# Kernel optimization log

Measured on AMD Instinct MI355X. Metric: run time of the kernel, lower is better.

Reference implementation:

```python
import jax, jax.numpy as jnp
import numpy as np

E = 19   # electrodes
H = 32   # lstm hidden dim per direction


def setup_inputs() -> dict:
    key = jax.random.key(0)
    ks = jax.random.split(key, 8)
    B, T = 64, 2048
    s = 1.0 / np.sqrt(H)  # PyTorch LSTM/Linear init scale
    u = lambda k, shp: jax.random.uniform(k, shp, jnp.float32, -s, s)
    return {
        "x": jax.random.normal(ks[0], (B, T, E), jnp.float32),
        # per-electrode, per-direction LSTM params (input_dim=1 so w_ih is a vector per gate block)
        "w_ih": u(ks[1], (E, 2, 4 * H)),          # [E, dir, 4H]
        "w_hh": u(ks[2], (E, 2, 4 * H, H)),       # [E, dir, 4H, H]
        "b_ih": u(ks[3], (E, 2, 4 * H)),
        "b_hh": u(ks[4], (E, 2, 4 * H)),
        "ln_gamma": jnp.ones((E, 2 * H), jnp.float32),
        "ln_beta": jnp.zeros((E, 2 * H), jnp.float32),
        "fc_w": u(ks[5], (1, 2 * H)),
        "fc_b": u(ks[6], (1,)),
    }


def reference(x, w_ih, w_hh, b_ih, b_hh, ln_gamma, ln_beta, fc_w, fc_b):
    B, T, E_ = x.shape
    # dir 0 = forward time, dir 1 = reversed time (bidirectional)
    xs = jnp.stack([x, x[:, ::-1, :]], axis=-1)      # [B, T, E, 2]
    xs = jnp.moveaxis(xs, 1, 0)                      # [T, B, E, 2]
    b = b_ih + b_hh                                  # [E, 2, 4H]

    h0 = jnp.zeros((B, E_, 2, H), x.dtype)
    c0 = jnp.zeros_like(h0)

    def step(carry, xt):
        h, c = carry
        # xt: [B, E, 2] scalar input per electrode/direction (input_dim == 1)
        gates = xt[..., None] * w_ih + jnp.einsum('bedh,edgh->bedg', h, w_hh) + b
        i, f, g, o = jnp.split(gates, 4, axis=-1)    # PyTorch gate order i,f,g,o
        c = jax.nn.sigmoid(f) * c + jax.nn.sigmoid(i) * jnp.tanh(g)
        h = jax.nn.sigmoid(o) * jnp.tanh(c)
        return (h, c), None

    (hT, _), _ = jax.lax.scan(step, (h0, c0), xs)
    # final hidden: dir0 = fwd at t=T-1 (hn[-2]), dir1 = bwd at t=0 (hn[-1]); concat features
    out = hT.reshape(B, E_, 2 * H)                   # [B, E, 64]

    # per-electrode LayerNorm over the 64-dim feature
    mu = out.mean(-1, keepdims=True)
    var = out.var(-1, keepdims=True)
    out = (out - mu) / jnp.sqrt(var + 1e-5) * ln_gamma + ln_beta

    pooled = out.mean(axis=1)                        # mean over electrodes -> [B, 64]
    logits = pooled @ fc_w.T + fc_b                  # [B, 1]
    return logits[:, 0]
```

## Files before the change

kernel.cpp:

```cpp
#include <hip/hip_runtime.h>
#include <math.h>
#include <stdint.h>

#define E_N 19
#define H_N 32
#define T_N 2048
#define B_N 64
#define G_N 128
#define XCHUNK 32
#define LOG2E 1.4426950408889634f

typedef _Float16 half2_t __attribute__((ext_vector_type(2)));

__device__ __forceinline__ float sigm_rcp(float e) {
    return __builtin_amdgcn_rcpf(1.0f + e);
}

__global__ __launch_bounds__(64)
__attribute__((amdgpu_waves_per_eu(1, 1)))
void lstm_chain_kernel(
    const float* __restrict__ x,
    const float* __restrict__ w_ih,
    const float* __restrict__ w_hh,
    const float* __restrict__ b_ih,
    const float* __restrict__ b_hh,
    float* __restrict__ hT)
{
    const int lane = threadIdx.x;
    const int be   = blockIdx.x;
    const int b    = be / E_N;
    const int e    = be - b * E_N;
    const int j    = lane & 31;
    const int half = lane >> 5;
    const int ed   = e * 2 + half;

    const float* wbase = w_hh + (size_t)ed * G_N * H_N;
    uint32_t wp[4][16];
    #pragma unroll
    for (int r = 0; r < 4; ++r) {
        const float* wr = wbase + (size_t)(j + 32 * r) * H_N;
        #pragma unroll
        for (int m = 0; m < 16; ++m) {
            float2 v = ((const float2*)wr)[m];
            half2_t p = { (_Float16)v.x, (_Float16)v.y };
            wp[r][m] = __builtin_bit_cast(uint32_t, p);
        }
    }
    float wih[4], bias[4];
    #pragma unroll
    for (int r = 0; r < 4; ++r) {
        const int row = j + 32 * r;
        wih[r]  = w_ih[(size_t)ed * G_N + row];
        bias[r] = b_ih[(size_t)ed * G_N + row] + b_hh[(size_t)ed * G_N + row];
    }

    __shared__ __align__(16) uint16_t hbuf[64];
    __shared__ float xbuf[64];

    hbuf[lane] = 0;
    float c = 0.0f, h = 0.0f;

    const float* xbase = x + (size_t)b * T_N * E_N + e;

    float xreg;
    {
        const int tphys = half ? (T_N - 1 - j) : j;
        xreg = xbase[(size_t)tphys * E_N];
    }

    for (int t0 = 0; t0 < T_N; t0 += XCHUNK) {
        #pragma unroll
        for (int r = 0; r < 4; ++r)
            #pragma unroll
            for (int m = 0; m < 16; ++m)
                asm volatile("" : "+v"(wp[r][m]));

        xbuf[lane] = xreg;
        if (t0 + XCHUNK < T_N) {
            const int tn    = t0 + XCHUNK + j;
            const int tphys = half ? (T_N - 1 - tn) : tn;
            xreg = xbase[(size_t)tphys * E_N];
        }

        #pragma unroll 1
        for (int tl = 0; tl < XCHUNK; ++tl) {
            const uint4 q0 = ((const uint4*)hbuf)[half * 4 + 0];
            const uint4 q1 = ((const uint4*)hbuf)[half * 4 + 1];
            const uint4 q2 = ((const uint4*)hbuf)[half * 4 + 2];
            const uint4 q3 = ((const uint4*)hbuf)[half * 4 + 3];
            const float sx = xbuf[(half << 5) + tl];

            uint32_t hp[16];
            hp[0]=q0.x; hp[1]=q0.y; hp[2]=q0.z; hp[3]=q0.w;
            hp[4]=q1.x; hp[5]=q1.y; hp[6]=q1.z; hp[7]=q1.w;
            hp[8]=q2.x; hp[9]=q2.y; hp[10]=q2.z; hp[11]=q2.w;
            hp[12]=q3.x; hp[13]=q3.y; hp[14]=q3.z; hp[15]=q3.w;

            float acc[4], accb[4];
            #pragma unroll
            for (int r = 0; r < 4; ++r) {
                acc[r]  = fmaf(sx, wih[r], bias[r]);
                accb[r] = 0.0f;
            }
            #pragma unroll
            for (int m = 0; m < 8; ++m) {
                #pragma unroll
                for (int r = 0; r < 4; ++r) {
                    acc[r]  = __builtin_amdgcn_fdot2(
                        __builtin_bit_cast(half2_t, hp[m]),
                        __builtin_bit_cast(half2_t, wp[r][m]),   acc[r],  false);
                    accb[r] = __builtin_amdgcn_fdot2(
                        __builtin_bit_cast(half2_t, hp[m + 8]),
                        __builtin_bit_cast(half2_t, wp[r][m + 8]), accb[r], false);
                }
            }
            const float gi = acc[0] + accb[0];
            const float gf = acc[1] + accb[1];
            const float gg = acc[2] + accb[2];
            const float go = acc[3] + accb[3];

            const float si = sigm_rcp(__builtin_amdgcn_exp2f(gi * (-LOG2E)));
            const float sf = sigm_rcp(__builtin_amdgcn_exp2f(gf * (-LOG2E)));
            const float tg = fmaf(2.0f, sigm_rcp(
                __builtin_amdgcn_exp2f(gg * (-2.0f * LOG2E))), -1.0f);
            const float so = sigm_rcp(__builtin_amdgcn_exp2f(go * (-LOG2E)));

            c = fmaf(sf, c, si * tg);
            const float tc = fmaf(2.0f, sigm_rcp(
                __builtin_amdgcn_exp2f(c * (-2.0f * LOG2E))), -1.0f);
            h = so * tc;

            hbuf[lane] = __builtin_bit_cast(uint16_t, (_Float16)h);
        }
    }

    hT[((size_t)(b * E_N + e) * 2 + half) * H_N + j] = h;
}

__global__ __launch_bounds__(64) void head_kernel(
    const float* __restrict__ hT,
    const float* __restrict__ ln_gamma,
    const float* __restrict__ ln_beta,
    const float* __restrict__ fc_w,
    const float* __restrict__ fc_b,
    float* __restrict__ out)
{
    const int b = blockIdx.x;
    const int f = threadIdx.x;

    float acc = 0.0f;
    for (int e = 0; e < E_N; ++e) {
        const float v = hT[(size_t)(b * E_N + e) * 64 + f];
        float s = v, s2 = v * v;
        #pragma unroll
        for (int off = 32; off > 0; off >>= 1) {
            s  += __shfl_xor(s,  off);
            s2 += __shfl_xor(s2, off);
        }
        const float mean = s * (1.0f / 64.0f);
        const float var  = s2 * (1.0f / 64.0f) - mean * mean;
        const float inv  = rsqrtf(var + 1e-5f);
        acc += (v - mean) * inv * ln_gamma[e * 64 + f] + ln_beta[e * 64 + f];
    }
    float contrib = (acc * (1.0f / (float)E_N)) * fc_w[f];
    #pragma unroll
    for (int off = 32; off > 0; off >>= 1) contrib += __shfl_xor(contrib, off);
    if (f == 0) out[b] = contrib + fc_b[0];
}

extern "C" void kernel_launch(void* const* d_in, const int* in_sizes, int n_in,
                              void* d_out, int out_size, void* d_ws, size_t ws_size,
                              hipStream_t stream) {
    const float* x        = (const float*)d_in[0];
    const float* w_ih     = (const float*)d_in[1];
    const float* w_hh     = (const float*)d_in[2];
    const float* b_ih     = (const float*)d_in[3];
    const float* b_hh     = (const float*)d_in[4];
    const float* ln_gamma = (const float*)d_in[5];
    const float* ln_beta  = (const float*)d_in[6];
    const float* fc_w     = (const float*)d_in[7];
    const float* fc_b     = (const float*)d_in[8];
    float* out = (float*)d_out;
    float* hT  = (float*)d_ws;

    lstm_chain_kernel<<<B_N * E_N, 64, 0, stream>>>(x, w_ih, w_hh, b_ih, b_hh, hT);
    head_kernel<<<B_N, 64, 0, stream>>>(hT, ln_gamma, ln_beta, fc_w, fc_b, out);
}
```

Before: 1.093 ms.

## Batch 16 sequences per wave and compute LSTM recurrence with MFMA

Replaces the per-(batch, electrode) fdot2 recurrence with one wave per (electrode, direction, group of 16 batches). The hidden-state matvec becomes eight 16x16x32 f16 MFMAs per step. The accumulator layout is arranged so each lane's new h values land directly in the B-fragment, which removes the LDS round trip for h. The gate activation scales are folded into the weights and bias. The grid shrinks from 1216 to 152 waves, so throughput now depends on per-step MFMA and transcendental latency rather than on how many waves can run at once. Each lane also computes 32 sigmoids per step instead of 4.

```diff
diff --git a/kernel.cpp b/kernel.cpp
--- a/kernel.cpp
+++ b/kernel.cpp
@@ -7,10 +7,10 @@
 #define T_N 2048
 #define B_N 64
 #define G_N 128
-#define XCHUNK 32
 #define LOG2E 1.4426950408889634f
 
-typedef _Float16 half2_t __attribute__((ext_vector_type(2)));
+typedef _Float16 f16x8 __attribute__((ext_vector_type(8)));
+typedef float    f32x4 __attribute__((ext_vector_type(4)));
 
 __device__ __forceinline__ float sigm_rcp(float e) {
     return __builtin_amdgcn_rcpf(1.0f + e);
@@ -18,7 +18,7 @@
 
 __global__ __launch_bounds__(64)
 __attribute__((amdgpu_waves_per_eu(1, 1)))
-void lstm_chain_kernel(
+void lstm_mfma_kernel(
     const float* __restrict__ x,
     const float* __restrict__ w_ih,
     const float* __restrict__ w_hh,
@@ -27,114 +27,104 @@
     float* __restrict__ hT)
 {
     const int lane = threadIdx.x;
-    const int be   = blockIdx.x;
-    const int b    = be / E_N;
-    const int e    = be - b * E_N;
-    const int j    = lane & 31;
-    const int half = lane >> 5;
-    const int ed   = e * 2 + half;
+    const int blk  = blockIdx.x;
+    const int ed   = blk >> 2;
+    const int g    = blk & 3;
+    const int e    = ed >> 1;
+    const int d    = ed & 1;
+    const int q    = lane >> 4;
+    const int col  = lane & 15;
+    const int b    = g * 16 + col;
 
-    const float* wbase = w_hh + (size_t)ed * G_N * H_N;
-    uint32_t wp[4][16];
+    const float* whh = w_hh + (size_t)ed * G_N * H_N;
+    f16x8 av[8];
+    float biasv[32], wihv[32];
     #pragma unroll
-    for (int r = 0; r < 4; ++r) {
-        const float* wr = wbase + (size_t)(j + 32 * r) * H_N;
+    for (int m = 0; m < 8; ++m) {
+        const float sc = ((m >> 1) == 2) ? (-2.0f * LOG2E) : (-LOG2E);
+        {
+            const int t   = col;
+            const int row = 32 * (m >> 1) + 8 * (t >> 2) + (t & 3) + 4 * (m & 1);
+            const float* wr = whh + (size_t)row * H_N + q * 8;
+            #pragma unroll
+            for (int j = 0; j < 8; ++j) av[m][j] = (_Float16)(wr[j] * sc);
+        }
         #pragma unroll
-        for (int m = 0; m < 16; ++m) {
-            float2 v = ((const float2*)wr)[m];
-            half2_t p = { (_Float16)v.x, (_Float16)v.y };
-            wp[r][m] = __builtin_bit_cast(uint32_t, p);
+        for (int r = 0; r < 4; ++r) {
+            const int row = 32 * (m >> 1) + 8 * q + r + 4 * (m & 1);
+            biasv[m * 4 + r] = (b_ih[(size_t)ed * G_N + row] +
+                                b_hh[(size_t)ed * G_N + row]) * sc;
+            wihv[m * 4 + r]  = w_ih[(size_t)ed * G_N + row] * sc;
         }
     }
-    float wih[4], bias[4];
+
+    float cst[8], hout[8];
+    f16x8 bfrag;
     #pragma unroll
-    for (int r = 0; r < 4; ++r) {
-        const int row = j + 32 * r;
-        wih[r]  = w_ih[(size_t)ed * G_N + row];
-        bias[r] = b_ih[(size_t)ed * G_N + row] + b_hh[(size_t)ed * G_N + row];
+    for (int dd = 0; dd < 8; ++dd) {
+        cst[dd] = 0.0f; hout[dd] = 0.0f; bfrag[dd] = (_Float16)0.0f;
     }
 
-    __shared__ __align__(16) uint16_t hbuf[64];
-    __shared__ float xbuf[64];
-
-    hbuf[lane] = 0;
-    float c = 0.0f, h = 0.0f;
-
-    const float* xbase = x + (size_t)b * T_N * E_N + e;
-
-    float xreg;
-    {
-        const int tphys = half ? (T_N - 1 - j) : j;
-        xreg = xbase[(size_t)tphys * E_N];
+    const float* xb = x + (size_t)b * T_N * E_N + e;
+    float xc[4], xn[4];
+    #pragma unroll
+    for (int s = 0; s < 4; ++s) {
+        const int tp = d ? (T_N - 1 - s) : s;
+        xc[s] = xb[(size_t)tp * E_N];
     }
 
-    for (int t0 = 0; t0 < T_N; t0 += XCHUNK) {
+    #pragma unroll 1
+    for (int t0 = 0; t0 < T_N; t0 += 4) {
+        if (t0 + 4 < T_N) {
+            #pragma unroll
+            for (int s = 0; s < 4; ++s) {
+                const int tn = t0 + 4 + s;
+                const int tp = d ? (T_N - 1 - tn) : tn;
+                xn[s] = xb[(size_t)tp * E_N];
+            }
+        }
         #pragma unroll
-        for (int r = 0; r < 4; ++r)
+        for (int s = 0; s < 4; ++s) {
+            const float xv = xc[s];
+            f32x4 C[8];
             #pragma unroll
-            for (int m = 0; m < 16; ++m)
-                asm volatile("" : "+v"(wp[r][m]));
-
-        xbuf[lane] = xreg;
-        if (t0 + XCHUNK < T_N) {
-            const int tn    = t0 + XCHUNK + j;
-            const int tphys = half ? (T_N - 1 - tn) : tn;
-            xreg = xbase[(size_t)tphys * E_N];
-        }
-
-        #pragma unroll 1
-        for (int tl = 0; tl < XCHUNK; ++tl) {
-            const uint4 q0 = ((const uint4*)hbuf)[half * 4 + 0];
-            const uint4 q1 = ((const uint4*)hbuf)[half * 4 + 1];
-            const uint4 q2 = ((const uint4*)hbuf)[half * 4 + 2];
-            const uint4 q3 = ((const uint4*)hbuf)[half * 4 + 3];
-            const float sx = xbuf[(half << 5) + tl];
-
-            uint32_t hp[16];
-            hp[0]=q0.x; hp[1]=q0.y; hp[2]=q0.z; hp[3]=q0.w;
-            hp[4]=q1.x; hp[5]=q1.y; hp[6]=q1.z; hp[7]=q1.w;
-            hp[8]=q2.x; hp[9]=q2.y; hp[10]=q2.z; hp[11]=q2.w;
-            hp[12]=q3.x; hp[13]=q3.y; hp[14]=q3.z; hp[15]=q3.w;
-
-            float acc[4], accb[4];
+            for (int m = 0; m < 8; ++m)
+                #pragma unroll
+                for (int r = 0; r < 4; ++r)
+                    C[m][r] = fmaf(wihv[m * 4 + r], xv, biasv[m * 4 + r]);
             #pragma unroll
-            for (int r = 0; r < 4; ++r) {
-                acc[r]  = fmaf(sx, wih[r], bias[r]);
-                accb[r] = 0.0f;
-            }
+            for (int m = 0; m < 8; ++m)
+                C[m] = __builtin_amdgcn_mfma_f32_16x16x32_f16(av[m], bfrag, C[m], 0, 0, 0);
             #pragma unroll
             for (int m = 0; m < 8; ++m) {
                 #pragma unroll
                 for (int r = 0; r < 4; ++r) {
-                    acc[r]  = __builtin_amdgcn_fdot2(
-                        __builtin_bit_cast(half2_t, hp[m]),
-                        __builtin_bit_cast(half2_t, wp[r][m]),   acc[r],  false);
-                    accb[r] = __builtin_amdgcn_fdot2(
-                        __builtin_bit_cast(half2_t, hp[m + 8]),
-                        __builtin_bit_cast(half2_t, wp[r][m + 8]), accb[r], false);
+                    const float sg = sigm_rcp(__builtin_amdgcn_exp2f(C[m][r]));
+                    C[m][r] = (m == 4 || m == 5) ? fmaf(2.0f, sg, -1.0f) : sg;
                 }
             }
-            const float gi = acc[0] + accb[0];
-            const float gf = acc[1] + accb[1];
-            const float gg = acc[2] + accb[2];
-            const float go = acc[3] + accb[3];
-
-            const float si = sigm_rcp(__builtin_amdgcn_exp2f(gi * (-LOG2E)));
-            const float sf = sigm_rcp(__builtin_amdgcn_exp2f(gf * (-LOG2E)));
-            const float tg = fmaf(2.0f, sigm_rcp(
-                __builtin_amdgcn_exp2f(gg * (-2.0f * LOG2E))), -1.0f);
-            const float so = sigm_rcp(__builtin_amdgcn_exp2f(go * (-LOG2E)));
-
-            c = fmaf(sf, c, si * tg);
-            const float tc = fmaf(2.0f, sigm_rcp(
-                __builtin_amdgcn_exp2f(c * (-2.0f * LOG2E))), -1.0f);
-            h = so * tc;
-
-            hbuf[lane] = __builtin_bit_cast(uint16_t, (_Float16)h);
+            #pragma unroll
+            for (int dd = 0; dd < 8; ++dd) {
+                const int hi = dd >> 2, r = dd & 3;
+                const float si = C[0 + hi][r];
+                const float sf = C[2 + hi][r];
+                const float tg = C[4 + hi][r];
+                const float so = C[6 + hi][r];
+                cst[dd] = fmaf(sf, cst[dd], si * tg);
+                const float tc = fmaf(2.0f, sigm_rcp(
+                    __builtin_amdgcn_exp2f(cst[dd] * (-2.0f * LOG2E))), -1.0f);
+                hout[dd] = so * tc;
+            }
+            #pragma unroll
+            for (int dd = 0; dd < 8; ++dd) bfrag[dd] = (_Float16)hout[dd];
         }
+        #pragma unroll
+        for (int s = 0; s < 4; ++s) xc[s] = xn[s];
     }
 
-    hT[((size_t)(b * E_N + e) * 2 + half) * H_N + j] = h;
+    float* dst = hT + (((size_t)(b * E_N + e)) * 2 + d) * H_N + 8 * q;
+    #pragma unroll
+    for (int dd = 0; dd < 8; ++dd) dst[dd] = hout[dd];
 }
 
 __global__ __launch_bounds__(64) void head_kernel(
@@ -183,6 +173,6 @@
     float* out = (float*)d_out;
     float* hT  = (float*)d_ws;
 
-    lstm_chain_kernel<<<B_N * E_N, 64, 0, stream>>>(x, w_ih, w_hh, b_ih, b_hh, hT);
+    lstm_mfma_kernel<<<E_N * 2 * 4, 64, 0, stream>>>(x, w_ih, w_hh, b_ih, b_hh, hT);
     head_kernel<<<B_N, 64, 0, stream>>>(hT, ln_gamma, ln_beta, fc_w, fc_b, out);
 }
```

Result: slower. 1.551 ms (+42.0%).
